# Performance work log

Measured on AMD Instinct MI355X. Metric: run time of the kernel, lower is better.

## Reference

```python
import jax, jax.numpy as jnp
import numpy as np

B, N, D, H = 8, 1024, 768, 12
HD = D // H


def setup_inputs() -> dict:
    key = jax.random.key(0)
    ks = jax.random.split(key, 9)
    s = 1.0 / np.sqrt(D)
    return {
        "x": jax.random.normal(ks[0], (B, N, D), dtype=jnp.float32),
        "Wq": jax.random.normal(ks[1], (D, D), dtype=jnp.float32) * s,
        "bq": jax.random.normal(ks[2], (D,), dtype=jnp.float32) * 0.01,
        "Wk": jax.random.normal(ks[3], (D, D), dtype=jnp.float32) * s,
        "bk": jax.random.normal(ks[4], (D,), dtype=jnp.float32) * 0.01,
        "Wv": jax.random.normal(ks[5], (D, D), dtype=jnp.float32) * s,
        "bv": jax.random.normal(ks[6], (D,), dtype=jnp.float32) * 0.01,
        "Wo": jax.random.normal(ks[7], (D, D), dtype=jnp.float32) * s,
        "bo": jax.random.normal(ks[8], (D,), dtype=jnp.float32) * 0.01,
    }


def reference(x, Wq, bq, Wk, bk, Wv, bv, Wo, bo):
    b, n, d = x.shape
    split = lambda t: t.reshape(b, n, H, HD).transpose(0, 2, 1, 3)  # b h n d
    q = split(x @ Wq + bq)
    k = split(x @ Wk + bk)
    v = split(x @ Wv + bv)
    energy = jnp.einsum('bhqd,bhkd->bhqk', q, k)
    # NOTE: module scales AFTER softmax by sqrt(emb_size) (not head_dim) -- faithful.
    att = jax.nn.softmax(energy, axis=-1) / jnp.sqrt(jnp.float32(D)).astype(x.dtype)
    out = jnp.einsum('bhqk,bhkd->bhqd', att, v)
    out = out.transpose(0, 2, 1, 3).reshape(b, n, d)
    return out @ Wo + bo
```

## Files before the change

### kernel.cpp

```cpp
#include <hip/hip_runtime.h>

#define B_  8
#define N_  1024
#define D_  768
#define H_  12
#define HD_ 64
#define M_  (B_ * N_)
#define WELEM (D_ * D_)
#define XELEM ((size_t)M_ * D_)

typedef _Float16 f16;
typedef f16   f16x8  __attribute__((ext_vector_type(8)));
typedef short bf16x8 __attribute__((ext_vector_type(8)));
typedef float f32x4  __attribute__((ext_vector_type(4)));
typedef unsigned short u16;

__device__ __forceinline__ u16 f2bf(float f) {
    unsigned int x = __float_as_uint(f);
    return (u16)((x + 0x7fffu + ((x >> 16) & 1u)) >> 16);
}
__device__ __forceinline__ float bf2f(u16 u) {
    return __uint_as_float(((unsigned int)u) << 16);
}
__device__ __forceinline__ u16 f2h(float f) {
    return __builtin_bit_cast(u16, (f16)f);
}

typedef __attribute__((address_space(3))) unsigned int       as3_u32;
typedef __attribute__((address_space(1))) const unsigned int as1_u32;
__device__ __forceinline__ void dma16(const void* g, void* l) {
    __builtin_amdgcn_global_load_lds((as1_u32*)g, (as3_u32*)l, 16, 0, 0);
}

__global__ __launch_bounds__(256) void cvt_x(const float* __restrict__ X,
                                             u16* __restrict__ Xh) {
    int idx = blockIdx.x * 256 + threadIdx.x;
    float4 v = ((const float4*)X)[idx];
    ushort4 o = {f2h(v.x), f2h(v.y), f2h(v.z), f2h(v.w)};
    ((ushort4*)Xh)[idx] = o;
}

__global__ __launch_bounds__(256) void cvt_w(
    const float* __restrict__ w0, const float* __restrict__ w1,
    const float* __restrict__ w2, const float* __restrict__ w3,
    u16* __restrict__ Wt) {
    const float* W = blockIdx.y == 0 ? w0 : blockIdx.y == 1 ? w1
                   : blockIdx.y == 2 ? w2 : w3;
    u16* dst = Wt + (size_t)blockIdx.y * WELEM;
    const int t  = threadIdx.x;
    const int tk = (blockIdx.x % 12) * 64, tn = (blockIdx.x / 12) * 64;
    __shared__ __align__(16) float tile[64][68];
#pragma unroll
    for (int i = 0; i < 4; ++i) {
        int r = (t >> 4) + i * 16, c4 = (t & 15) * 4;
        float4 v = *(const float4*)(W + (size_t)(tk + r) * D_ + tn + c4);
        *(float4*)&tile[r][c4] = v;
    }
    __syncthreads();
#pragma unroll
    for (int i = 0; i < 4; ++i) {
        int nr = (t >> 4) + i * 16, kc = (t & 15) * 4;
        ushort4 o = {f2h(tile[kc + 0][nr]), f2h(tile[kc + 1][nr]),
                     f2h(tile[kc + 2][nr]), f2h(tile[kc + 3][nr])};
        *(ushort4*)(dst + (size_t)(tn + nr) * D_ + tk + kc) = o;
    }
}

__global__ __launch_bounds__(256) void gemm_qkv(
    const u16* __restrict__ Xh, const u16* __restrict__ Wt,
    const float* __restrict__ bq, const float* __restrict__ bk,
    const float* __restrict__ bv, u16* __restrict__ Qf,
    u16* __restrict__ Kf, u16* __restrict__ Vt) {
    __shared__ __align__(16) u16 As[128 * 64];
    __shared__ __align__(16) u16 Bs[64 * 64];

    const int id  = blockIdx.x;
    const int xcd = id & 7, idx = id >> 3;
    const int m0  = (xcd * 8 + idx / 36) * 128;
    const int rem = idx % 36;
    const int z   = rem / 12, n0 = (rem % 12) * 64;

    const u16* Wz = Wt + (size_t)z * WELEM;
    const float* bias = z == 0 ? bq : z == 1 ? bk : bv;

    const int t = threadIdx.x, lane = t & 63, w = t >> 6;
    const int wm = w >> 1, wn = w & 1;
    const int quad = lane >> 4, ln = lane & 15;
    const int drow = lane >> 3, dcl = (lane & 7) ^ ((lane >> 3) & 7);

    f32x4 acc[4][2] = {};
    for (int k0 = 0; k0 < D_; k0 += 64) {
        __syncthreads();
#pragma unroll
        for (int j = 0; j < 4; ++j) {
            int i = w * 4 + j, row = i * 8 + drow;
            dma16(Xh + (size_t)(m0 + row) * D_ + k0 + dcl * 8, &As[i * 512]);
        }
#pragma unroll
        for (int j = 0; j < 2; ++j) {
            int i = w * 2 + j, row = i * 8 + drow;
            dma16(Wz + (size_t)(n0 + row) * D_ + k0 + dcl * 8, &Bs[i * 512]);
        }
        __syncthreads();
        f16x8 a[4][2], b[2][2];
#pragma unroll
        for (int mt = 0; mt < 4; ++mt)
#pragma unroll
            for (int ks = 0; ks < 2; ++ks)
                a[mt][ks] = *(const f16x8*)&As[(wm * 64 + mt * 16 + ln) * 64 +
                                               (((ks * 4 + quad) ^ (ln & 7)) * 8)];
#pragma unroll
        for (int nt = 0; nt < 2; ++nt)
#pragma unroll
            for (int ks = 0; ks < 2; ++ks)
                b[nt][ks] = *(const f16x8*)&Bs[(wn * 32 + nt * 16 + ln) * 64 +
                                               (((ks * 4 + quad) ^ (ln & 7)) * 8)];
#pragma unroll
        for (int mt = 0; mt < 4; ++mt)
#pragma unroll
            for (int nt = 0; nt < 2; ++nt) {
                acc[mt][nt] = __builtin_amdgcn_mfma_f32_16x16x32_f16(
                    a[mt][0], b[nt][0], acc[mt][nt], 0, 0, 0);
                acc[mt][nt] = __builtin_amdgcn_mfma_f32_16x16x32_f16(
                    a[mt][1], b[nt][1], acc[mt][nt], 0, 0, 0);
            }
    }
    const int h = n0 >> 6;
#pragma unroll
    for (int nt = 0; nt < 2; ++nt) {
        int hd = wn * 32 + nt * 16 + ln;
        float bv_ = bias[n0 + hd];
#pragma unroll
        for (int mt = 0; mt < 4; ++mt) {
            int mb = m0 + wm * 64 + mt * 16 + quad * 4;
            int bb = mb >> 10, ns = mb & 1023;
            if (z == 0) {
#pragma unroll
                for (int r = 0; r < 4; ++r)
                    Qf[(((size_t)bb * H_ + h) * N_ + ns + r) * HD_ + hd] =
                        f2h(acc[mt][nt][r] + bv_);
            } else if (z == 1) {
#pragma unroll
                for (int r = 0; r < 4; ++r)
                    Kf[(((size_t)bb * H_ + h) * N_ + ns + r) * HD_ + hd] =
                        f2h(acc[mt][nt][r] + bv_);
            } else {
                ushort4 o = {f2bf(acc[mt][nt][0] + bv_), f2bf(acc[mt][nt][1] + bv_),
                             f2bf(acc[mt][nt][2] + bv_), f2bf(acc[mt][nt][3] + bv_)};
                *(ushort4*)(Vt + (((size_t)bb * H_ + h) * HD_ + hd) * N_ + ns) = o;
            }
        }
    }
}

__global__ __launch_bounds__(256) void attn_mfma(
    const u16* __restrict__ Qg, const u16* __restrict__ Kg,
    const u16* __restrict__ Vtg, u16* __restrict__ Og) {
    __shared__ __align__(16) u16 Ks[64 * 64];
    __shared__ __align__(16) u16 Vs[64 * 64];
    __shared__ __align__(16) u16 Ps[128 * 72];

    const int t = threadIdx.x, lane = t & 63, w = t >> 6;
    const int quad = lane >> 4, ln = lane & 15;
    const int drow = lane >> 3, dcl = (lane & 7) ^ ((lane >> 3) & 7);
    const int id  = blockIdx.x;
    const int id2 = (id & 7) * 96 + (id >> 3);
    const int bh  = id2 >> 3, qt = id2 & 7;
    const u16* Qh  = Qg  + ((size_t)bh * N_ + qt * 128) * HD_;
    const u16* Kh  = Kg  + (size_t)bh * N_ * HD_;
    const u16* Vth = Vtg + (size_t)bh * HD_ * N_;
    u16*       Oh  = Og  + ((size_t)bh * N_ + qt * 128) * HD_;

    const int rho0 = (w * 2 + 0) * 8 + drow;
    const int rho1 = (w * 2 + 1) * 8 + drow;
    const int gk0  = 4 * (rho0 & 15) + (rho0 >> 4);
    const int gk1  = 4 * (rho1 & 15) + (rho1 >> 4);

    f16x8 aq[2][2];
#pragma unroll
    for (int mt = 0; mt < 2; ++mt)
#pragma unroll
        for (int ks = 0; ks < 2; ++ks)
            aq[mt][ks] = *(const f16x8*)(Qh + (size_t)(w * 32 + mt * 16 + ln) * HD_ +
                                         ks * 32 + quad * 8);

    float lsum[2][4] = {};
    f32x4 oacc[2][4] = {};

    for (int kt = 0; kt < 16; ++kt) {
        __syncthreads();
        dma16(Kh + (size_t)(kt * 64 + gk0) * HD_ + dcl * 8, &Ks[(w * 2 + 0) * 512]);
        dma16(Kh + (size_t)(kt * 64 + gk1) * HD_ + dcl * 8, &Ks[(w * 2 + 1) * 512]);
        dma16(Vth + (size_t)rho0 * N_ + kt * 64 + dcl * 8, &Vs[(w * 2 + 0) * 512]);
        dma16(Vth + (size_t)rho1 * N_ + kt * 64 + dcl * 8, &Vs[(w * 2 + 1) * 512]);
        __syncthreads();

        f32x4 sf[2][4];
#pragma unroll
        for (int nt = 0; nt < 4; ++nt) {
            f16x8 b0 = *(const f16x8*)&Ks[(nt * 16 + ln) * 64 + ((quad) ^ (ln & 7)) * 8];
            f16x8 b1 = *(const f16x8*)&Ks[(nt * 16 + ln) * 64 + ((4 + quad) ^ (ln & 7)) * 8];
#pragma unroll
            for (int mt = 0; mt < 2; ++mt) {
                f32x4 zz = {};
                sf[mt][nt] = __builtin_amdgcn_mfma_f32_16x16x32_f16(aq[mt][0], b0, zz, 0, 0, 0);
                sf[mt][nt] = __builtin_amdgcn_mfma_f32_16x16x32_f16(aq[mt][1], b1, sf[mt][nt], 0, 0, 0);
            }
        }

#pragma unroll
        for (int mt = 0; mt < 2; ++mt)
#pragma unroll
            for (int r = 0; r < 4; ++r) {
                unsigned int pu0 = f2bf(__expf(sf[mt][0][r] - 20.0f));
                unsigned int pu1 = f2bf(__expf(sf[mt][1][r] - 20.0f));
                unsigned int pu2 = f2bf(__expf(sf[mt][2][r] - 20.0f));
                unsigned int pu3 = f2bf(__expf(sf[mt][3][r] - 20.0f));
                uint2 pk;
                pk.x = pu0 | (pu1 << 16);
                pk.y = pu2 | (pu3 << 16);
                int q = w * 32 + mt * 16 + quad * 4 + r;
                *(uint2*)&Ps[q * 72 + ln * 4] = pk;
                lsum[mt][r] += bf2f((u16)pu0) + bf2f((u16)pu1) +
                               bf2f((u16)pu2) + bf2f((u16)pu3);
            }

#pragma unroll
        for (int mt = 0; mt < 2; ++mt) {
            bf16x8 ap0 = *(const bf16x8*)&Ps[(w * 32 + mt * 16 + ln) * 72 + quad * 8];
            bf16x8 ap1 = *(const bf16x8*)&Ps[(w * 32 + mt * 16 + ln) * 72 + 32 + quad * 8];
#pragma unroll
            for (int nt = 0; nt < 4; ++nt) {
                bf16x8 bv0 = *(const bf16x8*)&Vs[(nt * 16 + ln) * 64 +
                                                 ((quad ^ (ln & 7)) * 8)];
                oacc[mt][nt] = __builtin_amdgcn_mfma_f32_16x16x32_bf16(
                    ap0, bv0, oacc[mt][nt], 0, 0, 0);
                bf16x8 bv1 = *(const bf16x8*)&Vs[(nt * 16 + ln) * 64 +
                                                 (((4 + quad) ^ (ln & 7)) * 8)];
                oacc[mt][nt] = __builtin_amdgcn_mfma_f32_16x16x32_bf16(
                    ap1, bv1, oacc[mt][nt], 0, 0, 0);
            }
        }
    }

    const float sc = 0.036084391824351615f;
#pragma unroll
    for (int mt = 0; mt < 2; ++mt)
#pragma unroll
        for (int r = 0; r < 4; ++r) {
            float l = lsum[mt][r];
            l += __shfl_xor(l, 1);
            l += __shfl_xor(l, 2);
            l += __shfl_xor(l, 4);
            l += __shfl_xor(l, 8);
            float inv = sc / l;
#pragma unroll
            for (int nt = 0; nt < 4; ++nt)
                Oh[(size_t)(w * 32 + mt * 16 + quad * 4 + r) * HD_ + nt * 16 + ln] =
                    f2h(oacc[mt][nt][r] * inv);
        }
}

__global__ __launch_bounds__(256) void gemm_out(
    const u16* __restrict__ Ob, const u16* __restrict__ Wto,
    const float* __restrict__ bias, float* __restrict__ Out) {
    __shared__ __align__(16) u16 As[128 * 64];
    __shared__ __align__(16) u16 Bs[64 * 64];

    const int id  = blockIdx.x;
    const int id2 = (id & 7) * 96 + (id >> 3);
    const int m0  = (id2 / 12) * 128, n0 = (id2 % 12) * 64;

    const int t = threadIdx.x, lane = t & 63, w = t >> 6;
    const int wm = w >> 1, wn = w & 1;
    const int quad = lane >> 4, ln = lane & 15;
    const int drow = lane >> 3, dcl = (lane & 7) ^ ((lane >> 3) & 7);

    f32x4 acc[4][2] = {};
    for (int k0 = 0; k0 < D_; k0 += 64) {
        int head = k0 >> 6;
        __syncthreads();
#pragma unroll
        for (int j = 0; j < 4; ++j) {
            int i = w * 4 + j, row = i * 8 + drow;
            int m = m0 + row, bb = m >> 10, ns = m & 1023;
            dma16(Ob + (((size_t)bb * H_ + head) * N_ + ns) * HD_ + dcl * 8, &As[i * 512]);
        }
#pragma unroll
        for (int j = 0; j < 2; ++j) {
            int i = w * 2 + j, row = i * 8 + drow;
            dma16(Wto + (size_t)(n0 + row) * D_ + k0 + dcl * 8, &Bs[i * 512]);
        }
        __syncthreads();
        f16x8 a[4][2], b[2][2];
#pragma unroll
        for (int mt = 0; mt < 4; ++mt)
#pragma unroll
            for (int ks = 0; ks < 2; ++ks)
                a[mt][ks] = *(const f16x8*)&As[(wm * 64 + mt * 16 + ln) * 64 +
                                               (((ks * 4 + quad) ^ (ln & 7)) * 8)];
#pragma unroll
        for (int nt = 0; nt < 2; ++nt)
#pragma unroll
            for (int ks = 0; ks < 2; ++ks)
                b[nt][ks] = *(const f16x8*)&Bs[(wn * 32 + nt * 16 + ln) * 64 +
                                               (((ks * 4 + quad) ^ (ln & 7)) * 8)];
#pragma unroll
        for (int mt = 0; mt < 4; ++mt)
#pragma unroll
            for (int nt = 0; nt < 2; ++nt) {
                acc[mt][nt] = __builtin_amdgcn_mfma_f32_16x16x32_f16(
                    a[mt][0], b[nt][0], acc[mt][nt], 0, 0, 0);
                acc[mt][nt] = __builtin_amdgcn_mfma_f32_16x16x32_f16(
                    a[mt][1], b[nt][1], acc[mt][nt], 0, 0, 0);
            }
    }
#pragma unroll
    for (int nt = 0; nt < 2; ++nt) {
        int n = n0 + wn * 32 + nt * 16 + ln;
        float bv_ = bias[n];
#pragma unroll
        for (int mt = 0; mt < 4; ++mt) {
            int mb = m0 + wm * 64 + mt * 16 + quad * 4;
#pragma unroll
            for (int r = 0; r < 4; ++r)
                Out[(size_t)(mb + r) * D_ + n] = acc[mt][nt][r] + bv_;
        }
    }
}

extern "C" void kernel_launch(void* const* d_in, const int* in_sizes, int n_in,
                              void* d_out, int out_size, void* d_ws, size_t ws_size,
                              hipStream_t stream) {
    const float* x  = (const float*)d_in[0];
    const float* Wq = (const float*)d_in[1];
    const float* bq = (const float*)d_in[2];
    const float* Wk = (const float*)d_in[3];
    const float* bk = (const float*)d_in[4];
    const float* Wv = (const float*)d_in[5];
    const float* bv = (const float*)d_in[6];
    const float* Wo = (const float*)d_in[7];
    const float* bo = (const float*)d_in[8];

    u16* Xh = (u16*)d_ws;
    u16* Wt = Xh + XELEM;
    u16* Qf = Wt + 4 * (size_t)WELEM;
    u16* Kf = Qf + XELEM;
    u16* Vt = Kf + XELEM;
    u16* Ob = Vt + XELEM;

    cvt_x<<<dim3((int)(XELEM / 4 / 256)), 256, 0, stream>>>(x, Xh);
    cvt_w<<<dim3(144, 4), 256, 0, stream>>>(Wq, Wk, Wv, Wo, Wt);
    gemm_qkv<<<dim3(2304), 256, 0, stream>>>(Xh, Wt, bq, bk, bv, Qf, Kf, Vt);
    attn_mfma<<<dim3(768), 256, 0, stream>>>(Qf, Kf, Vt, Ob);
    gemm_out<<<dim3(768), 256, 0, stream>>>(
        Ob, Wt + 3 * (size_t)WELEM, bo, (float*)d_out);
}
```

Measured before the change: 206.2 us.

## Double-buffer K/V tiles in attention and use exp2 with packed bf16 conversion

The attention loop now prefetches the next K/V tile into a second LDS buffer with async global-to-LDS loads, using explicit vmcnt waits and barriers so the load overlaps the current tile's MFMA work. Q is pre-scaled by log2(e) in the projection kernel, so softmax can use the hardware exp2 and a rescaled bias. The manual bf16 rounding is replaced by the v_cvt_pk_bf16_f32 instruction. s_setprio hints raise wave priority around the MFMA sections. This costs twice the K/V LDS, which may lower occupancy, and relies on hand-written waitcnt counts being correct.

```diff
diff --git a/kernel.cpp b/kernel.cpp
--- a/kernel.cpp
+++ b/kernel.cpp
@@ -25,6 +25,19 @@
 __device__ __forceinline__ u16 f2h(float f) {
     return __builtin_bit_cast(u16, (f16)f);
 }
+__device__ __forceinline__ unsigned int cvtpk_bf16(float lo, float hi) {
+    unsigned int r;
+    asm("v_cvt_pk_bf16_f32 %0, %1, %2" : "=v"(r) : "v"(lo), "v"(hi));
+    return r;
+}
+#if __has_builtin(__builtin_amdgcn_exp2f)
+#define EXP2F(x) __builtin_amdgcn_exp2f(x)
+#else
+#define EXP2F(x) exp2f(x)
+#endif
+
+#define LOG2E_   1.4426950408889634f
+#define EXPBIAS_ 28.853900817779268f
 
 typedef __attribute__((address_space(3))) unsigned int       as3_u32;
 typedef __attribute__((address_space(1))) const unsigned int as1_u32;
@@ -138,7 +151,7 @@
 #pragma unroll
                 for (int r = 0; r < 4; ++r)
                     Qf[(((size_t)bb * H_ + h) * N_ + ns + r) * HD_ + hd] =
-                        f2h(acc[mt][nt][r] + bv_);
+                        f2h((acc[mt][nt][r] + bv_) * LOG2E_);
             } else if (z == 1) {
 #pragma unroll
                 for (int r = 0; r < 4; ++r)
@@ -156,8 +169,8 @@
 __global__ __launch_bounds__(256) void attn_mfma(
     const u16* __restrict__ Qg, const u16* __restrict__ Kg,
     const u16* __restrict__ Vtg, u16* __restrict__ Og) {
-    __shared__ __align__(16) u16 Ks[64 * 64];
-    __shared__ __align__(16) u16 Vs[64 * 64];
+    __shared__ __align__(16) u16 Ks[2][64 * 64];
+    __shared__ __align__(16) u16 Vs[2][64 * 64];
     __shared__ __align__(16) u16 Ps[128 * 72];
 
     const int t = threadIdx.x, lane = t & 63, w = t >> 6;
@@ -187,19 +200,33 @@
     float lsum[2][4] = {};
     f32x4 oacc[2][4] = {};
 
+    dma16(Kh + (size_t)(0 * 64 + gk0) * HD_ + dcl * 8, &Ks[0][(w * 2 + 0) * 512]);
+    dma16(Kh + (size_t)(0 * 64 + gk1) * HD_ + dcl * 8, &Ks[0][(w * 2 + 1) * 512]);
+    dma16(Vth + (size_t)rho0 * N_ + 0 * 64 + dcl * 8, &Vs[0][(w * 2 + 0) * 512]);
+    dma16(Vth + (size_t)rho1 * N_ + 0 * 64 + dcl * 8, &Vs[0][(w * 2 + 1) * 512]);
+
+#pragma unroll 2
     for (int kt = 0; kt < 16; ++kt) {
-        __syncthreads();
-        dma16(Kh + (size_t)(kt * 64 + gk0) * HD_ + dcl * 8, &Ks[(w * 2 + 0) * 512]);
-        dma16(Kh + (size_t)(kt * 64 + gk1) * HD_ + dcl * 8, &Ks[(w * 2 + 1) * 512]);
-        dma16(Vth + (size_t)rho0 * N_ + kt * 64 + dcl * 8, &Vs[(w * 2 + 0) * 512]);
-        dma16(Vth + (size_t)rho1 * N_ + kt * 64 + dcl * 8, &Vs[(w * 2 + 1) * 512]);
-        __syncthreads();
+        const int cur = kt & 1;
+        if (kt < 15) {
+            const int nk = (kt + 1) * 64;
+            dma16(Kh + (size_t)(nk + gk0) * HD_ + dcl * 8, &Ks[cur ^ 1][(w * 2 + 0) * 512]);
+            dma16(Kh + (size_t)(nk + gk1) * HD_ + dcl * 8, &Ks[cur ^ 1][(w * 2 + 1) * 512]);
+            dma16(Vth + (size_t)rho0 * N_ + nk + dcl * 8, &Vs[cur ^ 1][(w * 2 + 0) * 512]);
+            dma16(Vth + (size_t)rho1 * N_ + nk + dcl * 8, &Vs[cur ^ 1][(w * 2 + 1) * 512]);
+            asm volatile("s_waitcnt vmcnt(4)" ::: "memory");
+        } else {
+            asm volatile("s_waitcnt vmcnt(0)" ::: "memory");
+        }
+        __builtin_amdgcn_s_barrier();
+        __builtin_amdgcn_sched_barrier(0);
 
         f32x4 sf[2][4];
+        __builtin_amdgcn_s_setprio(1);
 #pragma unroll
         for (int nt = 0; nt < 4; ++nt) {
-            f16x8 b0 = *(const f16x8*)&Ks[(nt * 16 + ln) * 64 + ((quad) ^ (ln & 7)) * 8];
-            f16x8 b1 = *(const f16x8*)&Ks[(nt * 16 + ln) * 64 + ((4 + quad) ^ (ln & 7)) * 8];
+            f16x8 b0 = *(const f16x8*)&Ks[cur][(nt * 16 + ln) * 64 + ((quad) ^ (ln & 7)) * 8];
+            f16x8 b1 = *(const f16x8*)&Ks[cur][(nt * 16 + ln) * 64 + ((4 + quad) ^ (ln & 7)) * 8];
 #pragma unroll
             for (int mt = 0; mt < 2; ++mt) {
                 f32x4 zz = {};
@@ -207,40 +234,47 @@
                 sf[mt][nt] = __builtin_amdgcn_mfma_f32_16x16x32_f16(aq[mt][1], b1, sf[mt][nt], 0, 0, 0);
             }
         }
+        __builtin_amdgcn_s_setprio(0);
 
 #pragma unroll
         for (int mt = 0; mt < 2; ++mt)
 #pragma unroll
             for (int r = 0; r < 4; ++r) {
-                unsigned int pu0 = f2bf(__expf(sf[mt][0][r] - 20.0f));
-                unsigned int pu1 = f2bf(__expf(sf[mt][1][r] - 20.0f));
-                unsigned int pu2 = f2bf(__expf(sf[mt][2][r] - 20.0f));
-                unsigned int pu3 = f2bf(__expf(sf[mt][3][r] - 20.0f));
+                float e0 = EXP2F(sf[mt][0][r] - EXPBIAS_);
+                float e1 = EXP2F(sf[mt][1][r] - EXPBIAS_);
+                float e2 = EXP2F(sf[mt][2][r] - EXPBIAS_);
+                float e3 = EXP2F(sf[mt][3][r] - EXPBIAS_);
                 uint2 pk;
-                pk.x = pu0 | (pu1 << 16);
-                pk.y = pu2 | (pu3 << 16);
+                pk.x = cvtpk_bf16(e0, e1);
+                pk.y = cvtpk_bf16(e2, e3);
                 int q = w * 32 + mt * 16 + quad * 4 + r;
                 *(uint2*)&Ps[q * 72 + ln * 4] = pk;
-                lsum[mt][r] += bf2f((u16)pu0) + bf2f((u16)pu1) +
-                               bf2f((u16)pu2) + bf2f((u16)pu3);
-            }
-
+                lsum[mt][r] += __uint_as_float(pk.x << 16) +
+                               __uint_as_float(pk.x & 0xffff0000u) +
+                               __uint_as_float(pk.y << 16) +
+                               __uint_as_float(pk.y & 0xffff0000u);
+            }
+
+        __builtin_amdgcn_s_setprio(1);
 #pragma unroll
         for (int mt = 0; mt < 2; ++mt) {
             bf16x8 ap0 = *(const bf16x8*)&Ps[(w * 32 + mt * 16 + ln) * 72 + quad * 8];
             bf16x8 ap1 = *(const bf16x8*)&Ps[(w * 32 + mt * 16 + ln) * 72 + 32 + quad * 8];
 #pragma unroll
             for (int nt = 0; nt < 4; ++nt) {
-                bf16x8 bv0 = *(const bf16x8*)&Vs[(nt * 16 + ln) * 64 +
-                                                 ((quad ^ (ln & 7)) * 8)];
+                bf16x8 bv0 = *(const bf16x8*)&Vs[cur][(nt * 16 + ln) * 64 +
+                                                      ((quad ^ (ln & 7)) * 8)];
                 oacc[mt][nt] = __builtin_amdgcn_mfma_f32_16x16x32_bf16(
                     ap0, bv0, oacc[mt][nt], 0, 0, 0);
-                bf16x8 bv1 = *(const bf16x8*)&Vs[(nt * 16 + ln) * 64 +
-                                                 (((4 + quad) ^ (ln & 7)) * 8)];
+                bf16x8 bv1 = *(const bf16x8*)&Vs[cur][(nt * 16 + ln) * 64 +
+                                                      (((4 + quad) ^ (ln & 7)) * 8)];
                 oacc[mt][nt] = __builtin_amdgcn_mfma_f32_16x16x32_bf16(
                     ap1, bv1, oacc[mt][nt], 0, 0, 0);
             }
         }
+        __builtin_amdgcn_s_setprio(0);
+        __builtin_amdgcn_sched_barrier(0);
+        __builtin_amdgcn_s_barrier();
     }
 
     const float sc = 0.036084391824351615f;
```

Result: faster. 201.9 us (-2.1%).
